# Kernel tuning notes

Hardware: AMD Instinct MI355X
Metric: run time of the kernel (lower is better)

The kernel has to match this reference:

```python
import jax, jax.numpy as jnp
import numpy as np
from jax import lax

NUM_SEGMENTS = 50
HIDDEN = 128
IN_CH = 64
LOGSIG_DIM = IN_CH + IN_CH * (IN_CH - 1) // 2 + IN_CH  # level1 + Levy area + startpoint


def setup_inputs() -> dict:
    key = jax.random.key(0)
    k0, k1, k2, k3, k4 = jax.random.split(key, 5)
    B, C, T, V = 16, IN_CH, 200, 25
    x = jax.random.normal(k0, (B, C, T, V), dtype=jnp.float32)
    s = 1.0 / np.sqrt(HIDDEN).astype(np.float32)
    W_ih = jax.random.uniform(k1, (4 * HIDDEN, LOGSIG_DIM), jnp.float32, -s, s)
    W_hh = jax.random.uniform(k2, (4 * HIDDEN, HIDDEN), jnp.float32, -s, s)
    b_ih = jax.random.uniform(k3, (4 * HIDDEN,), jnp.float32, -s, s)
    b_hh = jax.random.uniform(k4, (4 * HIDDEN,), jnp.float32, -s, s)
    return {"x": x, "W_ih": W_ih, "W_hh": W_hh, "b_ih": b_ih, "b_hh": b_hh}


def _segment_logsig(xn):
    # xn: (N, C, T). Split T into NUM_SEGMENTS chunks; level-2 log-signature per chunk.
    N, C, T = xn.shape
    L = T // NUM_SEGMENTS  # points per segment
    p = xn.transpose(0, 2, 1).reshape(N, NUM_SEGMENTS, L, C)  # path points
    start = p[:, :, 0]                                  # (N,S,C) segment startpoint
    inc = p[:, :, 1:] - p[:, :, :-1]                    # (N,S,L-1,C) increments
    dev = p[:, :, :-1] - start[:, :, None]              # (N,S,L-1,C) p_t - p_0
    # Level-2 iterated integrals (cross terms): S2_ij = sum_t dev_t,i * inc_t,j
    S2 = jnp.einsum('nsti,nstj->nsij', dev, inc)        # (N,S,C,C)
    A = 0.5 * (S2 - S2.transpose(0, 1, 3, 2))           # Levy area (antisymmetric part)
    iu, ju = jnp.triu_indices(C, k=1)
    levy = A[:, :, iu, ju]                              # (N,S,C(C-1)/2)
    lvl1 = p[:, :, -1] - start                          # (N,S,C) level-1 term
    return jnp.concatenate([lvl1, levy, start], axis=-1)  # (N,S,LOGSIG_DIM)


def _lstm(seq, W_ih, W_hh, b_ih, b_hh):
    # seq: (N, S, F). Single-layer unidirectional LSTM, torch gate order (i,f,g,o).
    N = seq.shape[0]
    x_proj = jnp.einsum('nsf,gf->nsg', seq, W_ih) + b_ih + b_hh  # (N,S,4H)

    def step(carry, xt):
        h, c = carry
        gates = xt + h @ W_hh.T
        i, f, g, o = jnp.split(gates, 4, axis=-1)
        c = jax.nn.sigmoid(f) * c + jax.nn.sigmoid(i) * jnp.tanh(g)
        h = jax.nn.sigmoid(o) * jnp.tanh(c)
        return (h, c), h

    h0 = jnp.zeros((N, HIDDEN), seq.dtype)
    c0 = jnp.zeros((N, HIDDEN), seq.dtype)
    _, hs = lax.scan(step, (h0, c0), x_proj.transpose(1, 0, 2))
    return hs.transpose(1, 0, 2)  # (N,S,H)


def reference(x, W_ih, W_hh, b_ih, b_hh):
    B, C, T, V = x.shape
    xn = x.transpose(0, 3, 1, 2).reshape(B * V, C, T)
    ls = _segment_logsig(xn)                      # (B*V, S, LOGSIG_DIM)
    h = _lstm(ls, W_ih, W_hh, b_ih, b_hh)          # (B*V, S, H)
    out = h.reshape(B, V, NUM_SEGMENTS, HIDDEN).transpose(0, 3, 2, 1)
    return out  # (B, H, S, V)
```

## Files before the change

### kernel.cpp

```cpp
#include <hip/hip_runtime.h>
#include <stdint.h>

#define NSEG 50
#define HID 128
#define KDIM 2144
#define KD2 2240
#define KD2B 4480
#define NROW 20000
#define NROW_PAD 20224
#define GATES 512
#define NSEQ 400
#define NGRP 528

typedef __attribute__((ext_vector_type(8))) _Float16 f16x8;
typedef __attribute__((ext_vector_type(4))) _Float16 f16x4;
typedef __attribute__((ext_vector_type(4))) float f32x4;
typedef __attribute__((ext_vector_type(4))) uint32_t u32x4;

#define GLB_SPACE __attribute__((address_space(1)))
#define LDS_SPACE __attribute__((address_space(3)))

__device__ __forceinline__ void g2lds16(const void* g, void* l) {
    __builtin_amdgcn_global_load_lds((const GLB_SPACE uint32_t*)g,
                                     (LDS_SPACE uint32_t*)l, 16, 0, 0);
}

__device__ __forceinline__ int goff528(int i) {
    int n = 63 - i;
    int q = n >> 2, t = n & 3;
    return NGRP - (q + 1) * (2 * q + t);
}
__device__ __forceinline__ int ifromg(int g) {
    int i = 63 - (int)sqrtf(8.0f * (float)(NGRP - g));
    if (i < 0) i = 0;
    if (i > 62) i = 62;
    while (i > 0 && goff528(i) > g) i--;
    while (goff528(i + 1) <= g) i++;
    return i;
}

#define UVP(c) ((((c) & 3) << 4) | ((c) >> 2))

__global__ __launch_bounds__(512) void feat_kernel(const float* __restrict__ x,
                                                   const float* __restrict__ Wih,
                                                   const float* __restrict__ Whh,
                                                   const float* __restrict__ bih,
                                                   const float* __restrict__ bhh,
                                                   _Float16* __restrict__ feat,
                                                   _Float16* __restrict__ wh,
                                                   _Float16* __restrict__ whh16,
                                                   float* __restrict__ bias) {
    int bid = blockIdx.x;
    int tid = threadIdx.x;

    __shared__ float pbuf[64 * 101];
    __shared__ __align__(16) float4 uv4[25 * 64];

    if (bid >= 800) {
        int* kmap = (int*)pbuf;
        for (int k = tid; k < KD2; k += 512) {
            int orig;
            if (k < 64) {
                orig = k;
            } else if (k < 64 + 4 * NGRP) {
                int g = (k - 64) >> 2, p = (k - 64) & 3;
                int i = ifromg(g);
                int j = i + 1 + 4 * (g - goff528(i)) + p;
                orig = (j < 64) ? (64 + 63 * i - (i * (i - 1)) / 2 + (j - i - 1)) : -1;
            } else {
                orig = 2080 + (k - (64 + 4 * NGRP));
            }
            kmap[k] = orig;
        }
        __syncthreads();
        const int nwih = 512 * KD2;
        const int nwhh = 512 * HID;
        const int total = nwih + nwhh + 512;
        for (int idx = (bid - 800) * 512 + tid; idx < total; idx += 64 * 512) {
            if (idx < nwih) {
                int row = idx / KD2;
                int k = idx - row * KD2;
                int orig = kmap[k];
                wh[idx] = (orig >= 0) ? (_Float16)Wih[row * KDIM + orig] : (_Float16)0.0f;
            } else if (idx < nwih + nwhh) {
                int q = idx - nwih;
                whh16[q] = (_Float16)Whh[q];
            } else {
                int g = idx - nwih - nwhh;
                bias[g] = bih[g] + bhh[g];
            }
        }
        return;
    }

    int b = bid / NSEG;
    int s = bid - b * NSEG;

    for (int i = tid; i < 6400; i += 512) {
        int c = i / 100;
        int r = i - c * 100;
        pbuf[c * 101 + r] = x[(((size_t)b * 64 + c) * 200 + 4 * s) * 25 + r];
    }
    __syncthreads();

    for (int i = tid; i < 1600; i += 512) {
        int v = i >> 6;
        int c = i & 63;
        float p0 = pbuf[c * 101 + v];
        float p1 = pbuf[c * 101 + 25 + v];
        float p2 = pbuf[c * 101 + 50 + v];
        float p3 = pbuf[c * 101 + 75 + v];
        uv4[v * 64 + UVP(c)] = make_float4(p1 - p0, p2 - p0, p2 - p1, p3 - p2);
        size_t m = ((size_t)(b * 25 + v)) * NSEG + s;
        feat[m * KD2 + c] = (_Float16)(p3 - p0);
        feat[m * KD2 + (64 + 4 * NGRP) + c] = (_Float16)p0;
    }
    __syncthreads();

    for (int idx = tid; idx < 4 * NGRP; idx += 512) {
        int vb = idx / NGRP;
        int g = idx - vb * NGRP;
        int i = ifromg(g);
        int t = g - goff528(i);
        int j0 = i + 1 + 4 * t;
        int k0 = 64 + 4 * g;
        float msk[4];
        int jc[4];
#pragma unroll
        for (int p = 0; p < 4; p++) {
            int j = j0 + p;
            msk[p] = (j < 64) ? 0.5f : 0.0f;
            jc[p] = (j < 64) ? UVP(j) : UVP(63);
        }
        int ip = UVP(i);
        int v0 = (vb == 0) ? 0 : 6 * vb + 1;
        int vn = (vb == 0) ? 7 : 6;
        for (int vv = 0; vv < vn; vv++) {
            int v = v0 + vv;
            const float4* rowv = &uv4[v * 64];
            float4 a = rowv[ip];
            f16x4 o;
#pragma unroll
            for (int p = 0; p < 4; p++) {
                float4 bb = rowv[jc[p]];
                float val = msk[p] * (a.x * bb.z - bb.x * a.z + a.y * bb.w - bb.y * a.w);
                o[p] = (_Float16)val;
            }
            size_t m = ((size_t)(b * 25 + v)) * NSEG + s;
            *(f16x4*)(feat + m * KD2 + k0) = o;
        }
    }
}

__global__ __launch_bounds__(512, 2) void gemm_kernel(const _Float16* __restrict__ feat,
                                                      const _Float16* __restrict__ wh,
                                                      const float* __restrict__ bias,
                                                      _Float16* __restrict__ xproj2) {
    int bid = blockIdx.x;
    int mt = bid >> 1;
    int nb = bid & 1;
    int m0 = mt * 256;
    int n0 = nb * 256;
    int tid = threadIdx.x;
    int wave = tid >> 6;
    int lane = tid & 63;
    int quad = lane >> 4;
    int l15 = lane & 15;
    int wm = (wave >> 1) * 64;
    int wn = (wave & 1) * 128;

    int r8 = lane >> 3;
    int gcol = ((lane & 7) * 16) ^ (r8 * 16);

    __shared__ __align__(16) char smem[2][65536];

    const f32x4 z4 = {0.f, 0.f, 0.f, 0.f};
    f32x4 acc[4][8];
    for (int i = 0; i < 4; i++)
        for (int j = 0; j < 8; j++) acc[i][j] = z4;

    const char* featB = (const char*)feat;
    const char* whB = (const char*)wh;

    const char* aSrc[4];
    const char* bSrc[4];
#pragma unroll
    for (int it = 0; it < 4; it++) {
        int rb = it * 64 + wave * 8;
        aSrc[it] = featB + (size_t)(m0 + rb + r8) * KD2B + gcol;
        bSrc[it] = whB + (size_t)(n0 + rb + r8) * KD2B + gcol;
    }

    {
        char* As = smem[0];
        char* Bs = smem[0] + 32768;
#pragma unroll
        for (int it = 0; it < 4; it++) {
            int rb = it * 64 + wave * 8;
            g2lds16(aSrc[it], As + rb * 128);
            g2lds16(bSrc[it], Bs + rb * 128);
        }
    }
    __syncthreads();

    for (int kt = 0; kt < 35; kt++) {
        int cur = kt & 1;
        if (kt < 34) {
            size_t kb = (size_t)(kt + 1) * 128;
            char* As = smem[cur ^ 1];
            char* Bs = smem[cur ^ 1] + 32768;
#pragma unroll
            for (int it = 0; it < 4; it++) {
                int rb = it * 64 + wave * 8;
                g2lds16(aSrc[it] + kb, As + rb * 128);
                g2lds16(bSrc[it] + kb, Bs + rb * 128);
            }
        }
        {
            const char* As = smem[cur];
            const char* Bs = smem[cur] + 32768;
            for (int ks = 0; ks < 2; ks++) {
                int off = ((ks * 64) | (quad * 16)) ^ ((l15 & 7) * 16);
                f16x8 af[4], bf[8];
                for (int tt = 0; tt < 4; tt++)
                    af[tt] = *(const f16x8*)(As + (wm + tt * 16 + l15) * 128 + off);
                for (int tt = 0; tt < 8; tt++)
                    bf[tt] = *(const f16x8*)(Bs + (wn + tt * 16 + l15) * 128 + off);
                for (int mtl = 0; mtl < 4; mtl++)
                    for (int ntl = 0; ntl < 8; ntl++)
                        acc[mtl][ntl] = __builtin_amdgcn_mfma_f32_16x16x32_f16(af[mtl], bf[ntl], acc[mtl][ntl], 0, 0, 0);
            }
        }
        __syncthreads();
    }

    _Float16* ep = (_Float16*)smem;
    for (int p = 0; p < 2; p++) {
        if ((wave >> 2) == p) {
            for (int ntl = 0; ntl < 8; ntl++) {
                int nl = wn + ntl * 16 + l15;
                float bv = bias[n0 + nl];
                for (int mtl = 0; mtl < 4; mtl++)
                    for (int r = 0; r < 4; r++) {
                        int relm = wm - p * 128 + mtl * 16 + quad * 4 + r;
                        ep[relm * 260 + nl] = (_Float16)(acc[mtl][ntl][r] + bv);
                    }
            }
        }
        __syncthreads();
        for (int it = 0; it < 8; it++) {
            int rowp = it * 16 + (tid >> 5);
            int m = m0 + p * 128 + rowp;
            if (m < NROW) {
                unsigned q = (unsigned)m / 50u;
                unsigned s = (unsigned)m - q * 50u;
                const char* src = (const char*)ep + rowp * 520 + (tid & 31) * 16;
                char* dst = (char*)xproj2 + ((size_t)s * NSEQ + q) * 1024 + (size_t)n0 * 2 + (tid & 31) * 16;
                *(u32x4*)dst = *(const u32x4*)src;
            }
        }
        __syncthreads();
    }
}

__global__ __launch_bounds__(512, 2) void lstm_kernel(const _Float16* __restrict__ xproj2,
                                                      const _Float16* __restrict__ whh,
                                                      _Float16* __restrict__ hseq) {
    int bid = blockIdx.x;
    int tid = threadIdx.x;
    int wave = tid >> 6;
    int lane = tid & 63;
    int quad = lane >> 4;
    int col = lane & 15;
    int hid = wave * 16 + col;

    __shared__ __align__(16) char xbuf[25 * 4 * 1040];
    __shared__ __align__(16) _Float16 hst[NSEG * 4 * HID];
    __shared__ __align__(16) _Float16 hbuf[2][4 * 144];

    f16x8 bfrag[4][4];
    for (int g = 0; g < 4; g++) {
        int n = g * 128 + hid;
        for (int kq = 0; kq < 4; kq++)
            bfrag[g][kq] = *(const f16x8*)(whh + (size_t)n * HID + kq * 32 + quad * 8);
    }
    for (int i = tid; i < 2 * 4 * 144; i += 512) ((_Float16*)hbuf)[i] = (_Float16)0.0f;
    float cst = 0.0f;

    const char* xsrc = (const char*)xproj2;
    for (int r = wave; r < 100; r += 8)
        g2lds16(xsrc + ((size_t)((r >> 2) * NSEQ + bid * 4 + (r & 3))) * 1024 + lane * 16,
                xbuf + r * 1040);
    __syncthreads();

    const f32x4 z4 = {0.f, 0.f, 0.f, 0.f};
    for (int half = 0; half < 2; half++) {
        for (int ss = 0; ss < 25; ss++) {
            int s = half * 25 + ss;
            int cur = s & 1;
            int nxt = cur ^ 1;

            f16x8 afrag[4];
            for (int kq = 0; kq < 4; kq++)
                afrag[kq] = *(const f16x8*)(&hbuf[cur][(col & 3) * 144 + kq * 32 + quad * 8]);

            float xp[4];
            for (int g = 0; g < 4; g++)
                xp[g] = (float)(*(const _Float16*)(xbuf + (ss * 4 + quad) * 1040 +
                               (g * 128 + hid) * 2));

            f32x4 acc[4];
            for (int g = 0; g < 4; g++) {
                acc[g] = z4;
                for (int kq = 0; kq < 4; kq++)
                    acc[g] = __builtin_amdgcn_mfma_f32_16x16x32_f16(afrag[kq], bfrag[g][kq], acc[g], 0, 0, 0);
            }

            float gv[4];
            for (int g = 0; g < 4; g++) {
                float lo = (quad & 1) ? acc[g][1] : acc[g][0];
                float hi = (quad & 1) ? acc[g][3] : acc[g][2];
                gv[g] = (quad & 2) ? hi : lo;
            }

            float ip = gv[0] + xp[0];
            float fp = gv[1] + xp[1];
            float gp = gv[2] + xp[2];
            float op = gv[3] + xp[3];
            float si = __fdividef(1.0f, 1.0f + __expf(-ip));
            float sf = __fdividef(1.0f, 1.0f + __expf(-fp));
            float so = __fdividef(1.0f, 1.0f + __expf(-op));
            float eg = __expf(-2.0f * gp);
            float tg = __fdividef(1.0f - eg, 1.0f + eg);
            cst = sf * cst + si * tg;
            float ec = __expf(-2.0f * cst);
            float tc = __fdividef(1.0f - ec, 1.0f + ec);
            float hv = so * tc;
            _Float16 hv16 = (_Float16)hv;
            hbuf[nxt][quad * 144 + hid] = hv16;
            hst[(s * 4 + quad) * 128 + hid] = hv16;
            __syncthreads();
        }
        if (half == 0) {
            for (int r = wave; r < 100; r += 8)
                g2lds16(xsrc + ((size_t)((25 + (r >> 2)) * NSEQ + bid * 4 + (r & 3))) * 1024 + lane * 16,
                        xbuf + r * 1040);
            __syncthreads();
        }
    }

    const u32x4* src = (const u32x4*)hst;
    for (int i = tid; i < 3200; i += 512) {
        int s = i >> 6;
        int rem = i & 63;
        int seq = rem >> 4;
        int seg = rem & 15;
        u32x4 v = src[i];
        *(u32x4*)((char*)hseq + ((size_t)(s * NSEQ + bid * 4 + seq)) * 256 + seg * 16) = v;
    }
}

__global__ __launch_bounds__(256) void tr_kernel(const _Float16* __restrict__ hseq,
                                                 float* __restrict__ out) {
    int bid = blockIdx.x;
    int b = bid / NSEG;
    int s = bid - b * NSEG;
    int tid = threadIdx.x;

    __shared__ _Float16 buf[25 * 130];

    const uint32_t* src32 = (const uint32_t*)(hseq + ((size_t)s * NSEQ + b * 25) * HID);
    uint32_t* buf32 = (uint32_t*)buf;
    for (int i = tid; i < 1600; i += 256) {
        int v = i >> 6;
        int d = i & 63;
        buf32[v * 65 + d] = src32[i];
    }
    __syncthreads();
    for (int i = tid; i < 3200; i += 256) {
        int hid = i / 25;
        int v = i - hid * 25;
        out[(((size_t)b * 128 + hid) * NSEG + s) * 25 + v] = (float)buf[v * 130 + hid];
    }
}

extern "C" void kernel_launch(void* const* d_in, const int* in_sizes, int n_in,
                              void* d_out, int out_size, void* d_ws, size_t ws_size,
                              hipStream_t stream) {
    const float* x = (const float*)d_in[0];
    const float* Wih = (const float*)d_in[1];
    const float* Whh = (const float*)d_in[2];
    const float* bih = (const float*)d_in[3];
    const float* bhh = (const float*)d_in[4];
    float* out = (float*)d_out;

    char* ws = (char*)d_ws;
    size_t off = 0;
    _Float16* feat = (_Float16*)(ws + off);   off += (size_t)NROW_PAD * KD2 * 2;
    _Float16* xproj2 = (_Float16*)(ws + off); off += (size_t)NSEG * NSEQ * GATES * 2;
    _Float16* hseq = (_Float16*)(ws + off);   off += (size_t)NSEG * NSEQ * HID * 2;
    _Float16* wh = (_Float16*)(ws + off);     off += (size_t)512 * KD2 * 2;
    _Float16* whh16 = (_Float16*)(ws + off);  off += (size_t)512 * HID * 2;
    float* bias = (float*)(ws + off);         off += 512 * 4;

    hipLaunchKernelGGL(feat_kernel, dim3(864), dim3(512), 0, stream,
                       x, Wih, Whh, bih, bhh, feat, wh, whh16, bias);
    hipLaunchKernelGGL(gemm_kernel, dim3(158), dim3(512), 0, stream, feat, wh, bias, xproj2);
    hipLaunchKernelGGL(lstm_kernel, dim3(100), dim3(512), 0, stream, xproj2, whh16, hseq);
    hipLaunchKernelGGL(tr_kernel, dim3(16 * NSEG), dim3(256), 0, stream, hseq, out);
}
```

Before: 214.4 us.

## Deepen GEMM K-pipeline to four 32-wide LDS stages with vmcnt waits

```diff
diff --git a/kernel.cpp b/kernel.cpp
--- a/kernel.cpp
+++ b/kernel.cpp
@@ -169,10 +169,7 @@
     int wm = (wave >> 1) * 64;
     int wn = (wave & 1) * 128;
 
-    int r8 = lane >> 3;
-    int gcol = ((lane & 7) * 16) ^ (r8 * 16);
-
-    __shared__ __align__(16) char smem[2][65536];
+    __shared__ __align__(16) char lds[4][32768];
 
     const f32x4 z4 = {0.f, 0.f, 0.f, 0.f};
     f32x4 acc[4][8];
@@ -182,59 +179,63 @@
     const char* featB = (const char*)feat;
     const char* whB = (const char*)wh;
 
-    const char* aSrc[4];
-    const char* bSrc[4];
-#pragma unroll
-    for (int it = 0; it < 4; it++) {
-        int rb = it * 64 + wave * 8;
-        aSrc[it] = featB + (size_t)(m0 + rb + r8) * KD2B + gcol;
-        bSrc[it] = whB + (size_t)(n0 + rb + r8) * KD2B + gcol;
-    }
-
-    {
-        char* As = smem[0];
-        char* Bs = smem[0] + 32768;
-#pragma unroll
-        for (int it = 0; it < 4; it++) {
-            int rb = it * 64 + wave * 8;
-            g2lds16(aSrc[it], As + rb * 128);
-            g2lds16(bSrc[it], Bs + rb * 128);
-        }
-    }
+    int lr = lane >> 2;
+    int csw = (((lane & 3) ^ ((lane >> 3) & 3)) << 4);
+    const char* aU0 = featB + (size_t)(m0 + wave * 16 + lr) * KD2B + csw;
+    const char* aU1 = featB + (size_t)(m0 + (wave + 8) * 16 + lr) * KD2B + csw;
+    const char* bU0 = whB + (size_t)(n0 + wave * 16 + lr) * KD2B + csw;
+    const char* bU1 = whB + (size_t)(n0 + (wave + 8) * 16 + lr) * KD2B + csw;
+    int dA0 = wave * 1024;
+    int dA1 = (wave + 8) * 1024;
+    int dB0 = 16384 + wave * 1024;
+    int dB1 = 16384 + (wave + 8) * 1024;
+
+    int frsw = ((quad ^ ((l15 >> 1) & 3)) << 4);
+
+#define STAGE_HALF(h_) do {                                   \
+        char* Hb = lds[(h_) & 3];                             \
+        size_t kb = (size_t)(h_) * 64;                        \
+        g2lds16(aU0 + kb, Hb + dA0);                          \
+        g2lds16(aU1 + kb, Hb + dA1);                          \
+        g2lds16(bU0 + kb, Hb + dB0);                          \
+        g2lds16(bU1 + kb, Hb + dB1);                          \
+    } while (0)
+
+#define GPHASE(h_, VM, DO_STAGE) do {                                         \
+        if (DO_STAGE) STAGE_HALF((h_) + 3);                                   \
+        asm volatile("s_waitcnt vmcnt(" #VM ")" ::: "memory");                \
+        __builtin_amdgcn_s_barrier();                                         \
+        asm volatile("" ::: "memory");                                        \
+        const char* Hc = lds[(h_) & 3];                                       \
+        f16x8 af[4], bf[8];                                                   \
+        for (int tt = 0; tt < 4; tt++)                                        \
+            af[tt] = *(const f16x8*)(Hc + (wm + tt * 16 + l15) * 64 + frsw);  \
+        for (int tt = 0; tt < 8; tt++)                                        \
+            bf[tt] = *(const f16x8*)(Hc + 16384 + (wn + tt * 16 + l15) * 64 + frsw); \
+        __builtin_amdgcn_s_setprio(1);                                        \
+        for (int mtl = 0; mtl < 4; mtl++)                                     \
+            for (int ntl = 0; ntl < 8; ntl++)                                 \
+                acc[mtl][ntl] = __builtin_amdgcn_mfma_f32_16x16x32_f16(af[mtl], bf[ntl], acc[mtl][ntl], 0, 0, 0); \
+        __builtin_amdgcn_s_setprio(0);                                        \
+        asm volatile("" ::: "memory");                                        \
+        __builtin_amdgcn_s_barrier();                                         \
+    } while (0)
+
+    STAGE_HALF(0);
+    STAGE_HALF(1);
+    STAGE_HALF(2);
+
+    for (int h = 0; h < 67; h++) GPHASE(h, 12, true);
+    GPHASE(67, 8, false);
+    GPHASE(68, 4, false);
+    GPHASE(69, 0, false);
+
+#undef GPHASE
+#undef STAGE_HALF
+
     __syncthreads();
 
-    for (int kt = 0; kt < 35; kt++) {
-        int cur = kt & 1;
-        if (kt < 34) {
-            size_t kb = (size_t)(kt + 1) * 128;
-            char* As = smem[cur ^ 1];
-            char* Bs = smem[cur ^ 1] + 32768;
-#pragma unroll
-            for (int it = 0; it < 4; it++) {
-                int rb = it * 64 + wave * 8;
-                g2lds16(aSrc[it] + kb, As + rb * 128);
-                g2lds16(bSrc[it] + kb, Bs + rb * 128);
-            }
-        }
-        {
-            const char* As = smem[cur];
-            const char* Bs = smem[cur] + 32768;
-            for (int ks = 0; ks < 2; ks++) {
-                int off = ((ks * 64) | (quad * 16)) ^ ((l15 & 7) * 16);
-                f16x8 af[4], bf[8];
-                for (int tt = 0; tt < 4; tt++)
-                    af[tt] = *(const f16x8*)(As + (wm + tt * 16 + l15) * 128 + off);
-                for (int tt = 0; tt < 8; tt++)
-                    bf[tt] = *(const f16x8*)(Bs + (wn + tt * 16 + l15) * 128 + off);
-                for (int mtl = 0; mtl < 4; mtl++)
-                    for (int ntl = 0; ntl < 8; ntl++)
-                        acc[mtl][ntl] = __builtin_amdgcn_mfma_f32_16x16x32_f16(af[mtl], bf[ntl], acc[mtl][ntl], 0, 0, 0);
-            }
-        }
-        __syncthreads();
-    }
-
-    _Float16* ep = (_Float16*)smem;
+    _Float16* ep = (_Float16*)lds;
     for (int p = 0; p < 2; p++) {
         if ((wave >> 2) == p) {
             for (int ntl = 0; ntl < 8; ntl++) {
```

Result: slower. 225.0 us (+4.9%).
